# Optimization experiments

Measured on AMD Instinct MI355X. Metric: run time of the kernel, lower is better.

## Reference

```python
import jax, jax.numpy as jnp
import numpy as np

D = 1024      # n_embd
H = 2048      # expert_hidden_dim
G = 4         # num_groups
EPG = 2       # experts_per_group
NH = 16       # num_heads
HD = D // NH  # head dim
L = 4         # num_layers
V = 32000     # vocab_size
NC = 32000    # num_classes
MAXS = 2048   # max_seq_len
B, S = 2, 1024
TEMP = 1.0    # router_temperature


def setup_inputs() -> dict:
    key = jax.random.key(0)
    ks = jax.random.split(key, 12)
    sc = 0.02
    def n(k, shape):
        return jax.random.normal(k, shape, jnp.float32) * sc
    return {
        "x": jax.random.randint(ks[0], (B, S), 0, V),
        "tok_emb": n(ks[1], (V, D)),
        "pos_emb": n(ks[2], (MAXS, D)),
        "in_proj_w": n(ks[3], (L, 3 * D, D)),
        "in_proj_b": jnp.zeros((L, 3 * D)),
        "out_w": n(ks[4], (L, D, D)),
        "out_b": jnp.zeros((L, D)),
        "ln1_w": jnp.ones((L, D)), "ln1_b": jnp.zeros((L, D)),
        "ln2_w": jnp.ones((L, D)), "ln2_b": jnp.zeros((L, D)),
        "gr_w": n(ks[5], (L, D, G)), "gr_b": jnp.zeros((L, G)),
        "er_w": n(ks[6], (L, G, D, EPG)), "er_b": jnp.zeros((L, G, EPG)),
        "w1": n(ks[7], (L, G, EPG, D, H)), "b1": jnp.zeros((L, G, EPG, H)),
        "w2": n(ks[8], (L, G, EPG, H, D)), "b2": jnp.zeros((L, G, EPG, D)),
        "lnf_w": jnp.ones((D,)), "lnf_b": jnp.zeros((D,)),
        "head_w": n(ks[9], (NC, D)), "head_b": jnp.zeros((NC,)),
    }


def _ln(x, w, b):
    m = x.mean(-1, keepdims=True)
    v = ((x - m) ** 2).mean(-1, keepdims=True)
    return (x - m) * jax.lax.rsqrt(v + 1e-5) * w + b


def _attn(x, wqkv, bqkv, wo, bo, mask):
    b, s, _ = x.shape
    qkv = x @ wqkv.T + bqkv
    q, k, v = jnp.split(qkv, 3, axis=-1)
    def heads(t):
        return t.reshape(b, s, NH, HD).transpose(0, 2, 1, 3)
    q, k, v = heads(q), heads(k), heads(v)
    sc = jnp.einsum('bhqd,bhkd->bhqk', q, k) / np.float32(np.sqrt(HD))
    sc = jnp.where(mask, sc, jnp.float32(-1e30))
    a = jax.nn.softmax(sc, axis=-1)
    o = jnp.einsum('bhqk,bhkd->bhqd', a, v).transpose(0, 2, 1, 3).reshape(b, s, D)
    return o @ wo.T + bo


def _moe(x, gw, gb, ew, eb, w1, b1, w2, b2):
    # x: [T, D] flattened tokens. 2-level routing: top-1 group, top-1 expert in group.
    gp = jax.nn.softmax((x @ gw + gb) / TEMP, axis=-1)                      # [T,G]
    gidx = jnp.argmax(gp, axis=-1)                                          # [T]
    ep = jax.nn.softmax((jnp.einsum('td,gde->tge', x, ew) + eb) / TEMP, -1)  # [T,G,EPG]
    ep_sel = jnp.take_along_axis(ep, gidx[:, None, None], axis=1)[:, 0]     # [T,EPG]
    eidx = jnp.argmax(ep_sel, axis=-1)                                      # [T]
    gate = (jnp.take_along_axis(gp, gidx[:, None], 1)[:, 0]
            * jnp.take_along_axis(ep_sel, eidx[:, None], 1)[:, 0])          # [T]
    hmid = jax.nn.relu(jnp.einsum('td,gedh->tgeh', x, w1) + b1)             # [T,G,EPG,H]
    out = jnp.einsum('tgeh,gehd->tged', hmid, w2) + b2                      # [T,G,EPG,D]
    comb = (jax.nn.one_hot(gidx, G, dtype=x.dtype)[:, :, None]
            * jax.nn.one_hot(eidx, EPG, dtype=x.dtype)[:, None, :]) * gate[:, None, None]
    return jnp.einsum('tge,tged->td', comb, out)


def reference(x, tok_emb, pos_emb, in_proj_w, in_proj_b, out_w, out_b,
              ln1_w, ln1_b, ln2_w, ln2_b, gr_w, gr_b, er_w, er_b,
              w1, b1, w2, b2, lnf_w, lnf_b, head_w, head_b):
    b, s = x.shape
    h = tok_emb[x] + pos_emb[jnp.arange(s)][None]
    mask = jnp.tril(jnp.ones((s, s), bool))
    for l in range(L):
        x1 = _ln(h, ln1_w[l], ln1_b[l])
        h = h + _attn(x1, in_proj_w[l], in_proj_b[l], out_w[l], out_b[l], mask)
        x2 = _ln(h, ln2_w[l], ln2_b[l]).reshape(b * s, D)
        h = h + _moe(x2, gr_w[l], gr_b[l], er_w[l], er_b[l],
                     w1[l], b1[l], w2[l], b2[l]).reshape(b, s, D)
    h = _ln(h, lnf_w, lnf_b).mean(axis=1)
    return h @ head_w.T + head_b
```

## Files before the change

kernel.cpp:

```cpp
#include <hip/hip_runtime.h>
#include <hip/hip_bf16.h>
#include <cstdint>
#include <cstddef>

#define D_   1024
#define H_   2048
#define G_   4
#define EPG_ 2
#define NE_  8
#define NH_  16
#define HD_  64
#define L_   4
#define V_   32000
#define NC_  32000
#define B_   2
#define S_   1024
#define T_   2048
#define MAXBLK_ 40
#define QB_  128

typedef __attribute__((__ext_vector_type__(8))) __bf16 bf16x8;
typedef __attribute__((__ext_vector_type__(4))) __bf16 bf16x4;
typedef __attribute__((__ext_vector_type__(4))) float  f32x4;

__device__ __forceinline__ void gl_lds16(const void* g, void* l) {
  __builtin_amdgcn_global_load_lds(
      (const __attribute__((address_space(1))) void*)g,
      (__attribute__((address_space(3))) void*)l, 16, 0, 0);
}

__device__ __forceinline__ float wave_sum(float v) {
  #pragma unroll
  for (int o = 32; o >= 1; o >>= 1) v += __shfl_xor(v, o, 64);
  return v;
}

__global__ __launch_bounds__(256) void embed_kernel(const int* __restrict__ x,
    const float* __restrict__ tok, const float* __restrict__ pos,
    float* __restrict__ h) {
  int t = blockIdx.x;
  int tid = threadIdx.x;
  int token = x[t];
  int s = t & (S_ - 1);
  float4 tv = *(const float4*)(tok + (size_t)token * D_ + tid * 4);
  float4 pv = *(const float4*)(pos + (size_t)s * D_ + tid * 4);
  float4 r;
  r.x = tv.x + pv.x; r.y = tv.y + pv.y; r.z = tv.z + pv.z; r.w = tv.w + pv.w;
  *(float4*)(h + (size_t)t * D_ + tid * 4) = r;
}

__device__ __forceinline__ float block_sum256(float v, float* sbuf) {
  v = wave_sum(v);
  int tid = threadIdx.x;
  if ((tid & 63) == 0) sbuf[tid >> 6] = v;
  __syncthreads();
  float r = sbuf[0] + sbuf[1] + sbuf[2] + sbuf[3];
  __syncthreads();
  return r;
}

template<bool F32OUT, bool BFOUT>
__global__ __launch_bounds__(256) void ln_kernel(const float* __restrict__ X,
    const float* __restrict__ w, const float* __restrict__ b,
    float* __restrict__ Yf, __bf16* __restrict__ Yb) {
  __shared__ float sbuf[4];
  int t = blockIdx.x, tid = threadIdx.x;
  const float* xr = X + (size_t)t * D_;
  float4 v = *(const float4*)(xr + tid * 4);
  float sum = v.x + v.y + v.z + v.w;
  float m = block_sum256(sum, sbuf) * (1.0f / D_);
  float dx = v.x - m, dy = v.y - m, dz = v.z - m, dw = v.w - m;
  float vs = dx * dx + dy * dy + dz * dz + dw * dw;
  float var = block_sum256(vs, sbuf) * (1.0f / D_);
  float rs = rsqrtf(var + 1e-5f);
  float4 wv = *(const float4*)(w + tid * 4);
  float4 bv = *(const float4*)(b + tid * 4);
  float4 o;
  o.x = dx * rs * wv.x + bv.x;
  o.y = dy * rs * wv.y + bv.y;
  o.z = dz * rs * wv.z + bv.z;
  o.w = dw * rs * wv.w + bv.w;
  if (F32OUT) *(float4*)(Yf + (size_t)t * D_ + tid * 4) = o;
  if (BFOUT) {
    bf16x4 ob = {(__bf16)o.x, (__bf16)o.y, (__bf16)o.z, (__bf16)o.w};
    *(bf16x4*)(Yb + (size_t)t * D_ + tid * 4) = ob;
  }
}

__global__ __launch_bounds__(256) void ln_route_kernel(const float* __restrict__ X,
    const float* __restrict__ lw, const float* __restrict__ lb,
    const float* __restrict__ gw, const float* __restrict__ gb,
    const float* __restrict__ ew, const float* __restrict__ eb,
    __bf16* __restrict__ Yb, int* __restrict__ eidx, float* __restrict__ gate) {
  int wv = threadIdx.x >> 6, lane = threadIdx.x & 63;
  int t = blockIdx.x * 4 + wv;
  const float* xr = X + (size_t)t * D_;
  float4 xv[4];
  #pragma unroll
  for (int k = 0; k < 4; k++) xv[k] = *(const float4*)(xr + lane * 4 + k * 256);
  float s = 0.f;
  #pragma unroll
  for (int k = 0; k < 4; k++) s += xv[k].x + xv[k].y + xv[k].z + xv[k].w;
  float m = wave_sum(s) * (1.0f / D_);
  float vs = 0.f;
  #pragma unroll
  for (int k = 0; k < 4; k++) {
    float a = xv[k].x - m, b2 = xv[k].y - m, c = xv[k].z - m, d = xv[k].w - m;
    vs += a * a + b2 * b2 + c * c + d * d;
  }
  float rs = rsqrtf(wave_sum(vs) * (1.0f / D_) + 1e-5f);
  float y[4][4];
  #pragma unroll
  for (int k = 0; k < 4; k++) {
    int d0 = lane * 4 + k * 256;
    float4 wv4 = *(const float4*)(lw + d0);
    float4 bv4 = *(const float4*)(lb + d0);
    y[k][0] = (xv[k].x - m) * rs * wv4.x + bv4.x;
    y[k][1] = (xv[k].y - m) * rs * wv4.y + bv4.y;
    y[k][2] = (xv[k].z - m) * rs * wv4.z + bv4.z;
    y[k][3] = (xv[k].w - m) * rs * wv4.w + bv4.w;
    bf16x4 ob = {(__bf16)y[k][0], (__bf16)y[k][1], (__bf16)y[k][2], (__bf16)y[k][3]};
    *(bf16x4*)(Yb + (size_t)t * D_ + d0) = ob;
  }
  float g0 = 0, g1 = 0, g2 = 0, g3 = 0;
  #pragma unroll
  for (int k = 0; k < 4; k++)
    #pragma unroll
    for (int j = 0; j < 4; j++) {
      int d = lane * 4 + k * 256 + j;
      float4 gv = *(const float4*)(gw + (size_t)d * G_);
      float yv = y[k][j];
      g0 += yv * gv.x; g1 += yv * gv.y; g2 += yv * gv.z; g3 += yv * gv.w;
    }
  g0 = wave_sum(g0) + gb[0];
  g1 = wave_sum(g1) + gb[1];
  g2 = wave_sum(g2) + gb[2];
  g3 = wave_sum(g3) + gb[3];
  float mx = fmaxf(fmaxf(g0, g1), fmaxf(g2, g3));
  float p0 = __expf(g0 - mx), p1 = __expf(g1 - mx), p2 = __expf(g2 - mx), p3 = __expf(g3 - mx);
  float psum = p0 + p1 + p2 + p3;
  int gidx = 0; float best = g0;
  if (g1 > best) { best = g1; gidx = 1; }
  if (g2 > best) { best = g2; gidx = 2; }
  if (g3 > best) { best = g3; gidx = 3; }
  float gpsel = ((gidx == 0) ? p0 : (gidx == 1) ? p1 : (gidx == 2) ? p2 : p3) / psum;
  const float* ewg = ew + (size_t)gidx * D_ * EPG_;
  float e0 = 0, e1 = 0;
  #pragma unroll
  for (int k = 0; k < 4; k++)
    #pragma unroll
    for (int j = 0; j < 4; j++) {
      int d = lane * 4 + k * 256 + j;
      float2 ev = *(const float2*)(ewg + (size_t)d * EPG_);
      e0 += y[k][j] * ev.x; e1 += y[k][j] * ev.y;
    }
  e0 = wave_sum(e0) + eb[gidx * EPG_ + 0];
  e1 = wave_sum(e1) + eb[gidx * EPG_ + 1];
  float em = fmaxf(e0, e1);
  float q0 = __expf(e0 - em), q1 = __expf(e1 - em);
  int ei = (e1 > e0) ? 1 : 0;
  float epsel = ((ei == 0) ? q0 : q1) / (q0 + q1);
  if (lane == 0) {
    eidx[t] = gidx * EPG_ + ei;
    gate[t] = gpsel * epsel;
  }
}

__global__ __launch_bounds__(256) void finalize_kernel(const int* __restrict__ eidx,
    int* __restrict__ counts, int* __restrict__ offs, int* __restrict__ tlist,
    int* __restrict__ blk) {
  __shared__ int hist[256][NE_];
  __shared__ int eoff[NE_];
  int tid = threadIdx.x;
  int loc[NE_];
  #pragma unroll
  for (int e = 0; e < NE_; e++) loc[e] = 0;
  int te[8];
  #pragma unroll
  for (int i = 0; i < 8; i++) { te[i] = eidx[tid * 8 + i]; loc[te[i]]++; }
  #pragma unroll
  for (int e = 0; e < NE_; e++) hist[tid][e] = loc[e];
  __syncthreads();
  for (int off = 1; off < 256; off <<= 1) {
    int v[NE_];
    #pragma unroll
    for (int e = 0; e < NE_; e++) v[e] = (tid >= off) ? hist[tid - off][e] : 0;
    __syncthreads();
    #pragma unroll
    for (int e = 0; e < NE_; e++) hist[tid][e] += v[e];
    __syncthreads();
  }
  if (tid == 0) {
    int acc = 0, nb = 0;
    for (int e = 0; e < NE_; e++) {
      int c = hist[255][e];
      eoff[e] = acc; counts[e] = c; offs[e] = acc; acc += c;
      for (int mt = 0; mt * 64 < c; mt++) blk[nb++] = e | (mt << 8);
    }
    for (; nb < MAXBLK_; nb++) blk[nb] = -1;
  }
  __syncthreads();
  int run[NE_];
  #pragma unroll
  for (int e = 0; e < NE_; e++) run[e] = eoff[e] + hist[tid][e] - loc[e];
  #pragma unroll
  for (int i = 0; i < 8; i++) {
    int e = te[i];
    tlist[run[e]++] = tid * 8 + i;
  }
}

template<int MODE, int NF, bool KN>
__global__ __launch_bounds__(256, 3) void gemm_mfma(
    const __bf16* __restrict__ A, const float* __restrict__ W,
    const float* __restrict__ bias, float* __restrict__ Cf,
    __bf16* __restrict__ Cb, const int* __restrict__ tlist,
    const int* __restrict__ offs, const int* __restrict__ counts,
    const float* __restrict__ gate, const int* __restrict__ blk,
    int N, int K) {
  __shared__ __bf16 As[2][64 * 64];
  __shared__ __bf16 Bs[2][NF * 32 * 64];
  int e = 0, mt = blockIdx.y, cnt = T_;
  if (MODE >= 2) {
    int bv = blk[blockIdx.y];
    if (bv < 0) return;
    e = bv & 255; mt = bv >> 8;
    cnt = counts[e];
  }
  int row0 = mt * 64;
  int lbase = (MODE >= 2) ? offs[e] : 0;
  int col0 = blockIdx.x * (NF * 32);
  const float* Wp = W + (size_t)e * N * K;
  const float* bp = bias + (size_t)e * N;
  int tid = threadIdx.x;
  int w = tid >> 6, lane = tid & 63, lq = lane & 15, lg = lane >> 4;
  int wr = w >> 1, wc = w & 1;

  const __bf16* asrc[2];
  #pragma unroll
  for (int it = 0; it < 2; it++) {
    int v = it * 256 + tid;
    int r = v >> 3, u = v & 7;
    int gr = row0 + r;
    long rowidx;
    if (MODE == 2) rowidx = tlist[lbase + ((gr < cnt) ? gr : cnt - 1)];
    else if (MODE == 3) rowidx = lbase + ((gr < cnt) ? gr : cnt - 1);
    else rowidx = gr;
    asrc[it] = A + (size_t)rowidx * K + (u ^ (r & 7)) * 8;
  }
  const float* bsrc[NF];
  int bdst[NF];
  #pragma unroll
  for (int it = 0; it < NF; it++) {
    if (!KN) {
      int v = it * 256 + tid;
      int n = v >> 3, u = v & 7;
      bsrc[it] = Wp + (size_t)(col0 + n) * K + u * 8;
      bdst[it] = n * 64 + (u ^ (n & 7)) * 8;
    } else {
      int v = it * 256 + tid;
      int n = v & (NF * 32 - 1), u = v / (NF * 32);
      bsrc[it] = Wp + (size_t)(u * 8) * N + col0 + n;
      bdst[it] = n * 64 + (u ^ (n & 7)) * 8;
    }
  }

  float brp[NF * 8];
  f32x4 acc[2][NF] = {};

  auto loadB = [&](int k0) {
    #pragma unroll
    for (int it = 0; it < NF; it++) {
      if (!KN) {
        float4 f0 = *(const float4*)(bsrc[it] + k0);
        float4 f1 = *(const float4*)(bsrc[it] + k0 + 4);
        brp[it * 8 + 0] = f0.x; brp[it * 8 + 1] = f0.y;
        brp[it * 8 + 2] = f0.z; brp[it * 8 + 3] = f0.w;
        brp[it * 8 + 4] = f1.x; brp[it * 8 + 5] = f1.y;
        brp[it * 8 + 6] = f1.z; brp[it * 8 + 7] = f1.w;
      } else {
        #pragma unroll
        for (int j = 0; j < 8; j++)
          brp[it * 8 + j] = bsrc[it][(size_t)(k0 + j) * N];
      }
    }
  };
  auto writeB = [&](int buf) {
    #pragma unroll
    for (int it = 0; it < NF; it++) {
      bf16x8 bb = {(__bf16)brp[it * 8 + 0], (__bf16)brp[it * 8 + 1],
                   (__bf16)brp[it * 8 + 2], (__bf16)brp[it * 8 + 3],
                   (__bf16)brp[it * 8 + 4], (__bf16)brp[it * 8 + 5],
                   (__bf16)brp[it * 8 + 6], (__bf16)brp[it * 8 + 7]};
      *(bf16x8*)&Bs[buf][bdst[it]] = bb;
    }
  };
  auto stageA = [&](int buf, int k0) {
    #pragma unroll
    for (int it = 0; it < 2; it++)
      gl_lds16(asrc[it] + k0, &As[buf][(it * 256 + tid) * 8]);
  };
  auto mfmaPhase = [&](int buf) {
    __builtin_amdgcn_s_setprio(1);
    #pragma unroll
    for (int kk = 0; kk < 2; kk++) {
      bf16x8 a[2], b[NF];
      int us = ((lg + kk * 4) ^ (lq & 7)) * 8;
      #pragma unroll
      for (int fi = 0; fi < 2; fi++)
        a[fi] = *(const bf16x8*)&As[buf][(wr * 32 + fi * 16 + lq) * 64 + us];
      #pragma unroll
      for (int fj = 0; fj < NF; fj++)
        b[fj] = *(const bf16x8*)&Bs[buf][(wc * (NF * 16) + fj * 16 + lq) * 64 + us];
      #pragma unroll
      for (int fi = 0; fi < 2; fi++)
        #pragma unroll
        for (int fj = 0; fj < NF; fj++)
          acc[fi][fj] = __builtin_amdgcn_mfma_f32_16x16x32_bf16(a[fi], b[fj], acc[fi][fj], 0, 0, 0);
    }
    __builtin_amdgcn_s_setprio(0);
  };

  loadB(0);
  stageA(0, 0);
  writeB(0);
  __syncthreads();

  int buf = 0;
  for (int k0 = 0; k0 < K; k0 += 64) {
    int nk = k0 + 64;
    if (nk < K) {
      stageA(buf ^ 1, nk);
      loadB(nk);
    }
    mfmaPhase(buf);
    if (nk < K) writeB(buf ^ 1);
    __syncthreads();
    buf ^= 1;
  }

  #pragma unroll
  for (int fi = 0; fi < 2; fi++) {
    #pragma unroll
    for (int v = 0; v < 4; v++) {
      int r = row0 + wr * 32 + fi * 16 + lg * 4 + v;
      long orow;
      float gv = 1.f;
      if (MODE >= 2) {
        if (r >= cnt) continue;
        if (MODE == 2) orow = lbase + r;
        else { orow = tlist[lbase + r]; gv = gate[orow]; }
      } else {
        orow = r;
      }
      #pragma unroll
      for (int fj = 0; fj < NF; fj++) {
        int c = col0 + wc * (NF * 16) + fj * 16 + lq;
        float val = acc[fi][fj][v] + bp[c];
        if (MODE == 0)      Cb[orow * N + c] = (__bf16)val;
        else if (MODE == 1) Cf[orow * N + c] += val;
        else if (MODE == 2) Cb[orow * N + c] = (__bf16)fmaxf(val, 0.f);
        else                Cf[orow * N + c] += gv * val;
      }
    }
  }
}

#define SC_LOG2 0.18033688011112042f
__global__ __launch_bounds__(512) void attn_mfma_kernel(const __bf16* __restrict__ qkv,
                                                        __bf16* __restrict__ out) {
  __shared__ __bf16 Ks[2][64][72];
  __shared__ __bf16 Vt[2][64][72];
  __shared__ __bf16 Ps[QB_][72];
  int tid = threadIdx.x;
  int w = tid >> 6, lane = tid & 63, lq = lane & 15, lg = lane >> 4;
  int qt = (S_ / QB_ - 1) - blockIdx.x;
  int b = blockIdx.y >> 4, hh = blockIdx.y & 15;
  const __bf16* qbase = qkv + (size_t)b * S_ * 3 * D_ + hh * HD_;

  bf16x8 qa[2];
  {
    const __bf16* qp = qbase + (size_t)(qt * QB_ + w * 16 + lq) * 3 * D_ + lg * 8;
    qa[0] = *(const bf16x8*)qp;
    qa[1] = *(const bf16x8*)(qp + 32);
  }

  f32x4 o[4] = {};
  float m_[4] = {-1e30f, -1e30f, -1e30f, -1e30f};
  float l_[4] = {0.f, 0.f, 0.f, 0.f};

  int rowmin = qt * QB_ + w * 16;
  int srow = tid >> 3, sc8 = tid & 7;
  int nkt = qt * 2 + 2;

  auto stage = [&](int sb, int kt) {
    const __bf16* kp = qbase + (size_t)(kt * 64 + srow) * 3 * D_ + D_ + sc8 * 8;
    *(bf16x8*)&Ks[sb][srow][sc8 * 8] = *(const bf16x8*)kp;
    bf16x8 vv = *(const bf16x8*)(kp + D_);
    int cs = srow ^ (sc8 << 3);
    #pragma unroll
    for (int j = 0; j < 8; j++) Vt[sb][sc8 * 8 + j][cs] = vv[j];
  };

  stage(0, 0);
  __syncthreads();

  int buf = 0;
  for (int kt = 0; kt < nkt; kt++) {
    if (kt + 1 < nkt) stage(buf ^ 1, kt + 1);

    if (kt * 64 <= rowmin + 15) {
      f32x4 s[4] = {};
      #pragma unroll
      for (int kk = 0; kk < 2; kk++)
        #pragma unroll
        for (int fc = 0; fc < 4; fc++) {
          bf16x8 kf = *(const bf16x8*)&Ks[buf][fc * 16 + lq][lg * 8 + kk * 32];
          s[fc] = __builtin_amdgcn_mfma_f32_16x16x32_bf16(qa[kk], kf, s[fc], 0, 0, 0);
        }

      bool need_mask = (kt * 64 + 63 > rowmin);
      #pragma unroll
      for (int fc = 0; fc < 4; fc++)
        #pragma unroll
        for (int v = 0; v < 4; v++) {
          float sv = s[fc][v] * SC_LOG2;
          if (need_mask && (kt * 64 + fc * 16 + lq) > (rowmin + lg * 4 + v)) sv = -1e30f;
          s[fc][v] = sv;
        }

      #pragma unroll
      for (int v = 0; v < 4; v++) {
        float rm = fmaxf(fmaxf(s[0][v], s[1][v]), fmaxf(s[2][v], s[3][v]));
        #pragma unroll
        for (int o2 = 8; o2 >= 1; o2 >>= 1) rm = fmaxf(rm, __shfl_xor(rm, o2, 64));
        if (rm > m_[v]) {
          float cc = exp2f(m_[v] - rm);
          m_[v] = rm;
          l_[v] *= cc;
          o[0][v] *= cc; o[1][v] *= cc; o[2][v] *= cc; o[3][v] *= cc;
        }
        float rs = 0.f;
        #pragma unroll
        for (int fc = 0; fc < 4; fc++) {
          float p = exp2f(s[fc][v] - m_[v]);
          s[fc][v] = p; rs += p;
        }
        l_[v] += rs;
        #pragma unroll
        for (int fc = 0; fc < 4; fc++)
          Ps[w * 16 + lg * 4 + v][fc * 16 + lq] = (__bf16)s[fc][v];
      }
      asm volatile("" ::: "memory");

      #pragma unroll
      for (int kk = 0; kk < 2; kk++) {
        bf16x8 pa = *(const bf16x8*)&Ps[w * 16 + lq][lg * 8 + kk * 32];
        #pragma unroll
        for (int dc = 0; dc < 4; dc++) {
          int d = dc * 16 + lq;
          int col = (lg * 8 + kk * 32) ^ ((d >> 3) << 3);
          bf16x8 vb = *(const bf16x8*)&Vt[buf][d][col];
          o[dc] = __builtin_amdgcn_mfma_f32_16x16x32_bf16(pa, vb, o[dc], 0, 0, 0);
        }
      }
    }
    __syncthreads();
    buf ^= 1;
  }

  #pragma unroll
  for (int v = 0; v < 4; v++) {
    float ls = l_[v];
    #pragma unroll
    for (int o2 = 8; o2 >= 1; o2 >>= 1) ls += __shfl_xor(ls, o2, 64);
    float inv = 1.0f / ls;
    int row = rowmin + lg * 4 + v;
    __bf16* op = out + ((size_t)b * S_ + row) * D_ + hh * HD_;
    #pragma unroll
    for (int dc = 0; dc < 4; dc++)
      op[dc * 16 + lq] = (__bf16)(o[dc][v] * inv);
  }
}

__global__ __launch_bounds__(256) void mean_part_kernel(const float* __restrict__ X,
                                                        float* __restrict__ part) {
  int bd = blockIdx.x * 256 + threadIdx.x;
  int chunk = blockIdx.y;
  int b = bd >> 10, d = bd & 1023;
  float s = 0.f;
  #pragma unroll 4
  for (int i = 0; i < 64; i++) {
    int sidx = chunk * 64 + i;
    s += X[((size_t)b * S_ + sidx) * D_ + d];
  }
  part[chunk * T_ + bd] = s;
}

__global__ __launch_bounds__(256) void mean_final_kernel(const float* __restrict__ part,
                                                         float* __restrict__ hm) {
  int bd = blockIdx.x * 256 + threadIdx.x;
  float s = 0.f;
  #pragma unroll
  for (int c = 0; c < 16; c++) s += part[c * T_ + bd];
  hm[bd] = s * (1.0f / S_);
}

__global__ __launch_bounds__(256) void head_kernel(const float* __restrict__ hm,
    const float* __restrict__ hw, const float* __restrict__ hb,
    float* __restrict__ out) {
  int w = threadIdx.x >> 6;
  int lane = threadIdx.x & 63;
  int c = blockIdx.x * 4 + w;
  const float* row = hw + (size_t)c * D_;
  float acc0 = 0.f, acc1 = 0.f;
  #pragma unroll
  for (int k = 0; k < 4; k++) {
    int d = lane * 4 + k * 256;
    float4 wv = *(const float4*)(row + d);
    float4 h0 = *(const float4*)(hm + d);
    float4 h1 = *(const float4*)(hm + D_ + d);
    acc0 += wv.x * h0.x + wv.y * h0.y + wv.z * h0.z + wv.w * h0.w;
    acc1 += wv.x * h1.x + wv.y * h1.y + wv.z * h1.z + wv.w * h1.w;
  }
  #pragma unroll
  for (int o = 32; o >= 1; o >>= 1) {
    acc0 += __shfl_xor(acc0, o, 64);
    acc1 += __shfl_xor(acc1, o, 64);
  }
  if (lane == 0) {
    float bias = hb[c];
    out[c] = acc0 + bias;
    out[NC_ + c] = acc1 + bias;
  }
}

extern "C" void kernel_launch(void* const* d_in, const int* in_sizes, int n_in,
                              void* d_out, int out_size, void* d_ws, size_t ws_size,
                              hipStream_t stream) {
  const int*   x        = (const int*)d_in[0];
  const float* tok_emb  = (const float*)d_in[1];
  const float* pos_emb  = (const float*)d_in[2];
  const float* in_proj_w= (const float*)d_in[3];
  const float* in_proj_b= (const float*)d_in[4];
  const float* out_w    = (const float*)d_in[5];
  const float* out_b    = (const float*)d_in[6];
  const float* ln1_w    = (const float*)d_in[7];
  const float* ln1_b    = (const float*)d_in[8];
  const float* ln2_w    = (const float*)d_in[9];
  const float* ln2_b    = (const float*)d_in[10];
  const float* gr_w     = (const float*)d_in[11];
  const float* gr_b     = (const float*)d_in[12];
  const float* er_w     = (const float*)d_in[13];
  const float* er_b     = (const float*)d_in[14];
  const float* w1       = (const float*)d_in[15];
  const float* b1       = (const float*)d_in[16];
  const float* w2       = (const float*)d_in[17];
  const float* b2       = (const float*)d_in[18];
  const float* lnf_w    = (const float*)d_in[19];
  const float* lnf_b    = (const float*)d_in[20];
  const float* head_w   = (const float*)d_in[21];
  const float* head_b   = (const float*)d_in[22];

  char* wp = (char*)d_ws;
  auto carve = [&](size_t bytes) -> char* {
    char* p = wp;
    wp += (bytes + 255) & ~(size_t)255;
    return p;
  };
  float*  h      = (float*)carve((size_t)T_ * D_ * 4);
  float*  x1     = (float*)carve((size_t)T_ * D_ * 4);
  __bf16* x1b    = (__bf16*)carve((size_t)T_ * D_ * 2);
  __bf16* qkvb   = (__bf16*)carve((size_t)T_ * 3 * D_ * 2);
  __bf16* attnb  = (__bf16*)carve((size_t)T_ * D_ * 2);
  __bf16* hmidb  = (__bf16*)carve((size_t)T_ * H_ * 2);
  float*  part   = (float*)carve((size_t)16 * T_ * 4);
  float*  hm     = (float*)carve((size_t)B_ * D_ * 4);
  float*  gate   = (float*)carve((size_t)T_ * 4);
  int*    eidx   = (int*)carve((size_t)T_ * 4);
  int*    tlist  = (int*)carve((size_t)T_ * 4);
  int*    counts = (int*)carve(64);
  int*    offs   = (int*)carve(64);
  int*    blk    = (int*)carve(MAXBLK_ * 4);

  embed_kernel<<<T_, 256, 0, stream>>>(x, tok_emb, pos_emb, h);

  for (int l = 0; l < L_; l++) {
    ln_kernel<false, true><<<T_, 256, 0, stream>>>(h, ln1_w + l * D_, ln1_b + l * D_,
                                                   nullptr, x1b);
    gemm_mfma<0, 4, false><<<dim3(24, 32, 1), 256, 0, stream>>>(
        x1b, in_proj_w + (size_t)l * 3 * D_ * D_, in_proj_b + (size_t)l * 3 * D_,
        nullptr, qkvb, nullptr, nullptr, nullptr, nullptr, nullptr, 3 * D_, D_);
    attn_mfma_kernel<<<dim3(S_ / QB_, B_ * NH_), 512, 0, stream>>>(qkvb, attnb);
    gemm_mfma<1, 2, false><<<dim3(16, 32, 1), 256, 0, stream>>>(
        attnb, out_w + (size_t)l * D_ * D_, out_b + (size_t)l * D_, h, nullptr,
        nullptr, nullptr, nullptr, nullptr, nullptr, D_, D_);

    ln_route_kernel<<<T_ / 4, 256, 0, stream>>>(h,
        ln2_w + l * D_, ln2_b + l * D_,
        gr_w + (size_t)l * D_ * G_, gr_b + (size_t)l * G_,
        er_w + (size_t)l * G_ * D_ * EPG_, er_b + (size_t)l * G_ * EPG_,
        x1b, eidx, gate);
    finalize_kernel<<<1, 256, 0, stream>>>(eidx, counts, offs, tlist, blk);

    gemm_mfma<2, 4, true><<<dim3(H_ / 128, MAXBLK_, 1), 256, 0, stream>>>(
        x1b, w1 + (size_t)l * NE_ * D_ * H_, b1 + (size_t)l * NE_ * H_, nullptr, hmidb,
        tlist, offs, counts, nullptr, blk, H_, D_);
    gemm_mfma<3, 2, true><<<dim3(D_ / 64, MAXBLK_, 1), 256, 0, stream>>>(
        hmidb, w2 + (size_t)l * NE_ * H_ * D_, b2 + (size_t)l * NE_ * D_, h, nullptr,
        tlist, offs, counts, gate, blk, D_, H_);
  }

  ln_kernel<true, false><<<T_, 256, 0, stream>>>(h, lnf_w, lnf_b, x1, nullptr);
  mean_part_kernel<<<dim3(B_ * D_ / 256, 16), 256, 0, stream>>>(x1, part);
  mean_final_kernel<<<B_ * D_ / 256, 256, 0, stream>>>(part, hm);
  head_kernel<<<NC_ / 4, 256, 0, stream>>>(hm, head_w, head_b, (float*)d_out);
}
```

Baseline: 859.3 us.

## Remap GEMM workgroups across XCDs and shrink attention query tile to 64

```diff
diff --git a/kernel.cpp b/kernel.cpp
--- a/kernel.cpp
+++ b/kernel.cpp
@@ -17,7 +17,6 @@
 #define S_   1024
 #define T_   2048
 #define MAXBLK_ 40
-#define QB_  128
 
 typedef __attribute__((__ext_vector_type__(8))) __bf16 bf16x8;
 typedef __attribute__((__ext_vector_type__(4))) __bf16 bf16x4;
@@ -220,16 +219,23 @@
     int N, int K) {
   __shared__ __bf16 As[2][64 * 64];
   __shared__ __bf16 Bs[2][NF * 32 * 64];
-  int e = 0, mt = blockIdx.y, cnt = T_;
+
+  int gridX = gridDim.x;
+  int nwg = gridX * gridDim.y;
+  int flat = blockIdx.y * gridX + blockIdx.x;
+  int logical = ((nwg & 7) == 0) ? ((flat & 7) * (nwg >> 3) + (flat >> 3)) : flat;
+  int bx = logical % gridX, by = logical / gridX;
+
+  int e = 0, mt = by, cnt = T_;
   if (MODE >= 2) {
-    int bv = blk[blockIdx.y];
+    int bv = blk[by];
     if (bv < 0) return;
     e = bv & 255; mt = bv >> 8;
     cnt = counts[e];
   }
   int row0 = mt * 64;
   int lbase = (MODE >= 2) ? offs[e] : 0;
-  int col0 = blockIdx.x * (NF * 32);
+  int col0 = bx * (NF * 32);
   const float* Wp = W + (size_t)e * N * K;
   const float* bp = bias + (size_t)e * N;
   int tid = threadIdx.x;
@@ -367,20 +373,20 @@
 }
 
 #define SC_LOG2 0.18033688011112042f
-__global__ __launch_bounds__(512) void attn_mfma_kernel(const __bf16* __restrict__ qkv,
-                                                        __bf16* __restrict__ out) {
+__global__ __launch_bounds__(256, 3) void attn_mfma_kernel(const __bf16* __restrict__ qkv,
+                                                           __bf16* __restrict__ out) {
   __shared__ __bf16 Ks[2][64][72];
   __shared__ __bf16 Vt[2][64][72];
-  __shared__ __bf16 Ps[QB_][72];
+  __shared__ __bf16 Ps[64][72];
   int tid = threadIdx.x;
   int w = tid >> 6, lane = tid & 63, lq = lane & 15, lg = lane >> 4;
-  int qt = (S_ / QB_ - 1) - blockIdx.x;
+  int qt = (S_ / 64 - 1) - blockIdx.x;
   int b = blockIdx.y >> 4, hh = blockIdx.y & 15;
   const __bf16* qbase = qkv + (size_t)b * S_ * 3 * D_ + hh * HD_;
 
   bf16x8 qa[2];
   {
-    const __bf16* qp = qbase + (size_t)(qt * QB_ + w * 16 + lq) * 3 * D_ + lg * 8;
+    const __bf16* qp = qbase + (size_t)(qt * 64 + w * 16 + lq) * 3 * D_ + lg * 8;
     qa[0] = *(const bf16x8*)qp;
     qa[1] = *(const bf16x8*)(qp + 32);
   }
@@ -389,80 +395,81 @@
   float m_[4] = {-1e30f, -1e30f, -1e30f, -1e30f};
   float l_[4] = {0.f, 0.f, 0.f, 0.f};
 
-  int rowmin = qt * QB_ + w * 16;
-  int srow = tid >> 3, sc8 = tid & 7;
-  int nkt = qt * 2 + 2;
+  int rowmin = qt * 64 + w * 16;
 
   auto stage = [&](int sb, int kt) {
-    const __bf16* kp = qbase + (size_t)(kt * 64 + srow) * 3 * D_ + D_ + sc8 * 8;
-    *(bf16x8*)&Ks[sb][srow][sc8 * 8] = *(const bf16x8*)kp;
-    bf16x8 vv = *(const bf16x8*)(kp + D_);
-    int cs = srow ^ (sc8 << 3);
-    #pragma unroll
-    for (int j = 0; j < 8; j++) Vt[sb][sc8 * 8 + j][cs] = vv[j];
+    #pragma unroll
+    for (int it = 0; it < 2; it++) {
+      int idx = tid + it * 256;
+      int srow = idx >> 3, sc8 = idx & 7;
+      const __bf16* kp = qbase + (size_t)(kt * 64 + srow) * 3 * D_ + D_ + sc8 * 8;
+      *(bf16x8*)&Ks[sb][srow][sc8 * 8] = *(const bf16x8*)kp;
+      bf16x8 vv = *(const bf16x8*)(kp + D_);
+      int cs = srow ^ (sc8 << 3);
+      #pragma unroll
+      for (int j = 0; j < 8; j++) Vt[sb][sc8 * 8 + j][cs] = vv[j];
+    }
   };
 
   stage(0, 0);
   __syncthreads();
 
   int buf = 0;
-  for (int kt = 0; kt < nkt; kt++) {
-    if (kt + 1 < nkt) stage(buf ^ 1, kt + 1);
-
-    if (kt * 64 <= rowmin + 15) {
-      f32x4 s[4] = {};
-      #pragma unroll
-      for (int kk = 0; kk < 2; kk++)
-        #pragma unroll
-        for (int fc = 0; fc < 4; fc++) {
-          bf16x8 kf = *(const bf16x8*)&Ks[buf][fc * 16 + lq][lg * 8 + kk * 32];
-          s[fc] = __builtin_amdgcn_mfma_f32_16x16x32_bf16(qa[kk], kf, s[fc], 0, 0, 0);
-        }
-
-      bool need_mask = (kt * 64 + 63 > rowmin);
+  for (int kt = 0; kt <= qt; kt++) {
+    if (kt < qt) stage(buf ^ 1, kt + 1);
+
+    f32x4 s[4] = {};
+    #pragma unroll
+    for (int kk = 0; kk < 2; kk++)
+      #pragma unroll
+      for (int fc = 0; fc < 4; fc++) {
+        bf16x8 kf = *(const bf16x8*)&Ks[buf][fc * 16 + lq][lg * 8 + kk * 32];
+        s[fc] = __builtin_amdgcn_mfma_f32_16x16x32_bf16(qa[kk], kf, s[fc], 0, 0, 0);
+      }
+
+    bool need_mask = (kt == qt);
+    #pragma unroll
+    for (int fc = 0; fc < 4; fc++)
+      #pragma unroll
+      for (int v = 0; v < 4; v++) {
+        float sv = s[fc][v] * SC_LOG2;
+        if (need_mask && (fc * 16 + lq) > (w * 16 + lg * 4 + v)) sv = -1e30f;
+        s[fc][v] = sv;
+      }
+
+    #pragma unroll
+    for (int v = 0; v < 4; v++) {
+      float rm = fmaxf(fmaxf(s[0][v], s[1][v]), fmaxf(s[2][v], s[3][v]));
+      #pragma unroll
+      for (int o2 = 8; o2 >= 1; o2 >>= 1) rm = fmaxf(rm, __shfl_xor(rm, o2, 64));
+      if (rm > m_[v]) {
+        float cc = exp2f(m_[v] - rm);
+        m_[v] = rm;
+        l_[v] *= cc;
+        o[0][v] *= cc; o[1][v] *= cc; o[2][v] *= cc; o[3][v] *= cc;
+      }
+      float rs = 0.f;
+      #pragma unroll
+      for (int fc = 0; fc < 4; fc++) {
+        float p = exp2f(s[fc][v] - m_[v]);
+        s[fc][v] = p; rs += p;
+      }
+      l_[v] += rs;
       #pragma unroll
       for (int fc = 0; fc < 4; fc++)
-        #pragma unroll
-        for (int v = 0; v < 4; v++) {
-          float sv = s[fc][v] * SC_LOG2;
-          if (need_mask && (kt * 64 + fc * 16 + lq) > (rowmin + lg * 4 + v)) sv = -1e30f;
-          s[fc][v] = sv;
-        }
-
-      #pragma unroll
-      for (int v = 0; v < 4; v++) {
-        float rm = fmaxf(fmaxf(s[0][v], s[1][v]), fmaxf(s[2][v], s[3][v]));
-        #pragma unroll
-        for (int o2 = 8; o2 >= 1; o2 >>= 1) rm = fmaxf(rm, __shfl_xor(rm, o2, 64));
-        if (rm > m_[v]) {
-          float cc = exp2f(m_[v] - rm);
-          m_[v] = rm;
-          l_[v] *= cc;
-          o[0][v] *= cc; o[1][v] *= cc; o[2][v] *= cc; o[3][v] *= cc;
-        }
-        float rs = 0.f;
-        #pragma unroll
-        for (int fc = 0; fc < 4; fc++) {
-          float p = exp2f(s[fc][v] - m_[v]);
-          s[fc][v] = p; rs += p;
-        }
-        l_[v] += rs;
-        #pragma unroll
-        for (int fc = 0; fc < 4; fc++)
-          Ps[w * 16 + lg * 4 + v][fc * 16 + lq] = (__bf16)s[fc][v];
-      }
-      asm volatile("" ::: "memory");
-
-      #pragma unroll
-      for (int kk = 0; kk < 2; kk++) {
-        bf16x8 pa = *(const bf16x8*)&Ps[w * 16 + lq][lg * 8 + kk * 32];
-        #pragma unroll
-        for (int dc = 0; dc < 4; dc++) {
-          int d = dc * 16 + lq;
-          int col = (lg * 8 + kk * 32) ^ ((d >> 3) << 3);
-          bf16x8 vb = *(const bf16x8*)&Vt[buf][d][col];
-          o[dc] = __builtin_amdgcn_mfma_f32_16x16x32_bf16(pa, vb, o[dc], 0, 0, 0);
-        }
+        Ps[w * 16 + lg * 4 + v][fc * 16 + lq] = (__bf16)s[fc][v];
+    }
+    asm volatile("" ::: "memory");
+
+    #pragma unroll
+    for (int kk = 0; kk < 2; kk++) {
+      bf16x8 pa = *(const bf16x8*)&Ps[w * 16 + lq][lg * 8 + kk * 32];
+      #pragma unroll
+      for (int dc = 0; dc < 4; dc++) {
+        int d = dc * 16 + lq;
+        int col = (lg * 8 + kk * 32) ^ ((d >> 3) << 3);
+        bf16x8 vb = *(const bf16x8*)&Vt[buf][d][col];
+        o[dc] = __builtin_amdgcn_mfma_f32_16x16x32_bf16(pa, vb, o[dc], 0, 0, 0);
       }
     }
     __syncthreads();
@@ -591,7 +598,7 @@
     gemm_mfma<0, 4, false><<<dim3(24, 32, 1), 256, 0, stream>>>(
         x1b, in_proj_w + (size_t)l * 3 * D_ * D_, in_proj_b + (size_t)l * 3 * D_,
         nullptr, qkvb, nullptr, nullptr, nullptr, nullptr, nullptr, 3 * D_, D_);
-    attn_mfma_kernel<<<dim3(S_ / QB_, B_ * NH_), 512, 0, stream>>>(qkvb, attnb);
+    attn_mfma_kernel<<<dim3(S_ / 64, B_ * NH_), 256, 0, stream>>>(qkvb, attnb);
     gemm_mfma<1, 2, false><<<dim3(16, 32, 1), 256, 0, stream>>>(
         attnb, out_w + (size_t)l * D_ * D_, out_b + (size_t)l * D_, h, nullptr,
         nullptr, nullptr, nullptr, nullptr, nullptr, D_, D_);
```

Result: no change. 869.4 us (+1.2%).
